# Kernel optimization log

Hardware: AMD Instinct MI355X
Metric: run time of the kernel (lower is better)

The kernel has to match this reference:

```python
import jax, jax.numpy as jnp
import numpy as np

B, N, D = 64, 50000, 64


def setup_inputs() -> dict:
    key = jax.random.key(0)
    k1, k2 = jax.random.split(key)
    q = jax.random.normal(k1, (B, D), dtype=jnp.float32)
    X = jax.random.normal(k2, (N, D), dtype=jnp.float32)
    feature_weights = jnp.ones((D,), dtype=jnp.float32)  # nn.Parameter init
    return {"q": q, "X": X, "feature_weights": feature_weights}


def reference(q, X, feature_weights):
    # w = softplus(feature_weights), then weighted L1 distance:
    # dist[b, n] = sum_d w[d] * |q[b, d] - X[n, d]|
    w = jax.nn.softplus(feature_weights)  # [D]
    # broadcast abs-diff [B, N, D] reduced over D (the implicit cdist tensor)
    diff = jnp.abs(q[:, None, :] - X[None, :, :])  # [B, N, D]
    dist = jnp.einsum("bnd,d->bn", diff, w)  # [B, N]
    return dist
```

## Files before the change

kernel.cpp:

```cpp
#include <hip/hip_runtime.h>
#include <math.h>


constexpr int D = 64;
constexpr int BCHUNK = 16;
constexpr int NT = 256;
constexpr int ROWS = 256;
constexpr int CH = 64;
constexpr int PAD = 68;

__global__ __launch_bounds__(NT, 3)
void fdist_kernel(const float* __restrict__ q,
                  const float* __restrict__ X,
                  const float* __restrict__ fw,
                  float* __restrict__ out, int N) {
    __shared__ float ws[D];
    __shared__ float qs[BCHUNK][D];
    __shared__ float xtile[CH][PAD];

    const int t = threadIdx.x;
    const int wave = t >> 6;
    const int lane = t & 63;

    const int nwg = gridDim.x;
    const int orig = blockIdx.x;
    const int q8 = nwg >> 3, r8 = nwg & 7;
    const int xcd = orig & 7, pos = orig >> 3;
    const int wg = (xcd < r8 ? xcd * (q8 + 1) : r8 * (q8 + 1) + (xcd - r8) * q8) + pos;
    const int xb = wg >> 2;
    const int yb = wg & 3;
    const int bbase = yb * BCHUNK;
    const int nbase = xb * ROWS;
    const int n = nbase + t;

    const int rsub = t >> 4;
    const int col  = t & 15;
    const float4* Xv = reinterpret_cast<const float4*>(X);

    float4 buf[2][4];
#pragma unroll
    for (int jj = 0; jj < 4; ++jj) {
        int grow = nbase + jj * 16 + rsub;
        grow = grow < N ? grow : N - 1;
        buf[0][jj] = Xv[(size_t)grow * 16 + col];
    }
#pragma unroll
    for (int jj = 0; jj < 4; ++jj) {
        int grow = nbase + CH + jj * 16 + rsub;
        grow = grow < N ? grow : N - 1;
        buf[1][jj] = Xv[(size_t)grow * 16 + col];
    }

    if (t < D) {
        float x = fw[t];
        ws[t] = fmaxf(x, 0.f) + log1pf(expf(-fabsf(x)));
    }
    __syncthreads();

#pragma unroll
    for (int i = t; i < BCHUNK * D; i += NT) {
        qs[i >> 6][i & (D - 1)] = ws[i & (D - 1)] * q[(size_t)bbase * D + i];
    }

    const float4 wv = *reinterpret_cast<const float4*>(&ws[col * 4]);

    float4 xs[16];
#pragma unroll
    for (int c = 0; c < 4; ++c) {
#pragma unroll
        for (int jj = 0; jj < 4; ++jj) {
            float4 v = buf[c & 1][jj];
            v.x *= wv.x; v.y *= wv.y; v.z *= wv.z; v.w *= wv.w;
            *reinterpret_cast<float4*>(&xtile[jj * 16 + rsub][col * 4]) = v;
        }
        if (c + 2 < 4) {
#pragma unroll
            for (int jj = 0; jj < 4; ++jj) {
                int grow = nbase + (c + 2) * CH + jj * 16 + rsub;
                grow = grow < N ? grow : N - 1;
                buf[c & 1][jj] = Xv[(size_t)grow * 16 + col];
            }
        }
        __syncthreads();
        if (wave == c) {
#pragma unroll
            for (int i = 0; i < 16; ++i)
                xs[i] = *reinterpret_cast<const float4*>(&xtile[lane][i * 4]);
        }
        __syncthreads();
    }

#pragma unroll
    for (int bi = 0; bi < BCHUNK; ++bi) {
        float ax = 0.f, ay = 0.f, az = 0.f, aw = 0.f;
#pragma unroll
        for (int i = 0; i < 16; ++i) {
            const float4 qv = *reinterpret_cast<const float4*>(&qs[bi][4 * i]);
            ax += fabsf(qv.x - xs[i].x);
            ay += fabsf(qv.y - xs[i].y);
            az += fabsf(qv.z - xs[i].z);
            aw += fabsf(qv.w - xs[i].w);
        }
        if (n < N) out[(size_t)(bbase + bi) * N + n] = (ax + ay) + (az + aw);
    }
}

extern "C" void kernel_launch(void* const* d_in, const int* in_sizes, int n_in,
                              void* d_out, int out_size, void* d_ws, size_t ws_size,
                              hipStream_t stream) {
    const float* q  = (const float*)d_in[0];
    const float* X  = (const float*)d_in[1];
    const float* fw = (const float*)d_in[2];
    float* out = (float*)d_out;

    const int B = in_sizes[0] / D;
    const int N = in_sizes[1] / D;

    const int nxblk = (N + ROWS - 1) / ROWS;
    const int nwg = nxblk * (B / BCHUNK);
    fdist_kernel<<<dim3(nwg), dim3(NT), 0, stream>>>(q, X, fw, out, N);
}
```

Measured before the change: 22.01 us.

## Split weight prep into separate kernel and drop block-wide barriers in distance kernel

Moves the softplus weights and weighted-q computation into a tiny prep kernel that writes to workspace, so the main kernel reads q rows directly from global/scalar memory instead of shared memory. The main kernel drops to 128 threads and 128 rows per block, and each wave stages its own 64 rows into a swizzled LDS tile, so block-wide __syncthreads are replaced by a per-wave waitcnt. The bi loop is only partially unrolled. This adds an extra kernel launch and serial dependency, and relies on per-wave LDS ownership for correctness without a barrier.

Measured after the change: 44.81 us. +103.6%, slower.

```diff
diff --git a/kernel.cpp b/kernel.cpp
--- a/kernel.cpp
+++ b/kernel.cpp
@@ -4,19 +4,30 @@
 
 constexpr int D = 64;
 constexpr int BCHUNK = 16;
-constexpr int NT = 256;
-constexpr int ROWS = 256;
-constexpr int CH = 64;
-constexpr int PAD = 68;
+constexpr int NT = 128;
+constexpr int ROWS = 128;
 
-__global__ __launch_bounds__(NT, 3)
-void fdist_kernel(const float* __restrict__ q,
-                  const float* __restrict__ X,
-                  const float* __restrict__ fw,
-                  float* __restrict__ out, int N) {
+__global__ void prep_kernel(const float* __restrict__ q,
+                            const float* __restrict__ fw,
+                            float* __restrict__ wq, int B) {
     __shared__ float ws[D];
-    __shared__ float qs[BCHUNK][D];
-    __shared__ float xtile[CH][PAD];
+    const int t = threadIdx.x;
+    if (t < D) {
+        float x = fw[t];
+        float w = fmaxf(x, 0.f) + log1pf(expf(-fabsf(x)));
+        ws[t] = w;
+        wq[B * D + t] = w;
+    }
+    __syncthreads();
+    for (int i = t; i < B * D; i += blockDim.x)
+        wq[i] = ws[i & (D - 1)] * q[i];
+}
+
+__global__ __launch_bounds__(NT, 4)
+void fdist_kernel(const float* __restrict__ X,
+                  const float* __restrict__ wq,
+                  float* __restrict__ out, int N, int wsoff4) {
+    __shared__ float4 xq[ROWS * 16];
 
     const int t = threadIdx.x;
     const int wave = t >> 6;
@@ -28,74 +39,41 @@
     const int xcd = orig & 7, pos = orig >> 3;
     const int wg = (xcd < r8 ? xcd * (q8 + 1) : r8 * (q8 + 1) + (xcd - r8) * q8) + pos;
     const int xb = wg >> 2;
-    const int yb = wg & 3;
-    const int bbase = yb * BCHUNK;
+    const int bbase = (wg & 3) * BCHUNK;
     const int nbase = xb * ROWS;
-    const int n = nbase + t;
 
-    const int rsub = t >> 4;
-    const int col  = t & 15;
+    const int rsub = lane >> 4;
+    const int col = lane & 15;
     const float4* Xv = reinterpret_cast<const float4*>(X);
+    const float4* wq4 = reinterpret_cast<const float4*>(wq);
 
-    float4 buf[2][4];
-#pragma unroll
-    for (int jj = 0; jj < 4; ++jj) {
-        int grow = nbase + jj * 16 + rsub;
-        grow = grow < N ? grow : N - 1;
-        buf[0][jj] = Xv[(size_t)grow * 16 + col];
-    }
-#pragma unroll
-    for (int jj = 0; jj < 4; ++jj) {
-        int grow = nbase + CH + jj * 16 + rsub;
-        grow = grow < N ? grow : N - 1;
-        buf[1][jj] = Xv[(size_t)grow * 16 + col];
-    }
-
-    if (t < D) {
-        float x = fw[t];
-        ws[t] = fmaxf(x, 0.f) + log1pf(expf(-fabsf(x)));
-    }
-    __syncthreads();
+    const float4 wv = wq4[wsoff4 + col];
 
 #pragma unroll
-    for (int i = t; i < BCHUNK * D; i += NT) {
-        qs[i >> 6][i & (D - 1)] = ws[i & (D - 1)] * q[(size_t)bbase * D + i];
+    for (int j = 0; j < 16; ++j) {
+        const int r = j * 4 + rsub;
+        int grow = nbase + wave * 64 + r;
+        grow = grow < N ? grow : N - 1;
+        float4 v = Xv[(size_t)grow * 16 + col];
+        v.x *= wv.x; v.y *= wv.y; v.z *= wv.z; v.w *= wv.w;
+        xq[(wave * 64 + r) * 16 + (col ^ (r & 7))] = v;
     }
-
-    const float4 wv = *reinterpret_cast<const float4*>(&ws[col * 4]);
+    asm volatile("s_waitcnt vmcnt(0) lgkmcnt(0)" ::: "memory");
 
     float4 xs[16];
 #pragma unroll
-    for (int c = 0; c < 4; ++c) {
-#pragma unroll
-        for (int jj = 0; jj < 4; ++jj) {
-            float4 v = buf[c & 1][jj];
-            v.x *= wv.x; v.y *= wv.y; v.z *= wv.z; v.w *= wv.w;
-            *reinterpret_cast<float4*>(&xtile[jj * 16 + rsub][col * 4]) = v;
-        }
-        if (c + 2 < 4) {
-#pragma unroll
-            for (int jj = 0; jj < 4; ++jj) {
-                int grow = nbase + (c + 2) * CH + jj * 16 + rsub;
-                grow = grow < N ? grow : N - 1;
-                buf[c & 1][jj] = Xv[(size_t)grow * 16 + col];
-            }
-        }
-        __syncthreads();
-        if (wave == c) {
-#pragma unroll
-            for (int i = 0; i < 16; ++i)
-                xs[i] = *reinterpret_cast<const float4*>(&xtile[lane][i * 4]);
-        }
-        __syncthreads();
-    }
+    for (int i = 0; i < 16; ++i)
+        xs[i] = xq[(wave * 64 + lane) * 16 + (i ^ (lane & 7))];
 
-#pragma unroll
+    const int n = nbase + wave * 64 + lane;
+
+#pragma unroll 4
     for (int bi = 0; bi < BCHUNK; ++bi) {
+        const float4* qrow = wq4 + (size_t)(bbase + bi) * 16;
         float ax = 0.f, ay = 0.f, az = 0.f, aw = 0.f;
 #pragma unroll
         for (int i = 0; i < 16; ++i) {
-            const float4 qv = *reinterpret_cast<const float4*>(&qs[bi][4 * i]);
+            const float4 qv = qrow[i];
             ax += fabsf(qv.x - xs[i].x);
             ay += fabsf(qv.y - xs[i].y);
             az += fabsf(qv.z - xs[i].z);
@@ -112,11 +90,14 @@
     const float* X  = (const float*)d_in[1];
     const float* fw = (const float*)d_in[2];
     float* out = (float*)d_out;
+    float* wq = (float*)d_ws;
 
     const int B = in_sizes[0] / D;
     const int N = in_sizes[1] / D;
 
+    prep_kernel<<<dim3(1), dim3(256), 0, stream>>>(q, fw, wq, B);
+
     const int nxblk = (N + ROWS - 1) / ROWS;
     const int nwg = nxblk * (B / BCHUNK);
-    fdist_kernel<<<dim3(nwg), dim3(NT), 0, stream>>>(q, X, fw, out, N);
+    fdist_kernel<<<dim3(nwg), dim3(NT), 0, stream>>>(X, wq, out, N, B * D / 4);
 }
```
